# Kernel tuning notes

Measured on AMD Instinct MI355X. Metric: run time of the kernel, lower is better.

The kernel has to match this reference:

```python
import jax, jax.numpy as jnp
import numpy as np

S, B, I, H = 2048, 64, 128, 128
E = float(np.e)


def setup_inputs() -> dict:
    key = jax.random.key(0)
    ks = jax.random.split(key, 16)
    s = 1.0 / np.sqrt(H)
    inp = {
        "x": jax.random.normal(ks[0], (S, B, I), jnp.float32),
        "h0": jnp.zeros((2, B, H), jnp.float32),
        "c0": jnp.zeros((2, B, H), jnp.float32),
        # elapsed times, strictly positive
        "delta_ts": jax.random.uniform(ks[1], (B, S), jnp.float32, 0.1, 10.0),
    }
    names = ["W_ih", "W_hh", "b_ih", "b_hh", "W_d", "b_d"]
    shapes = [(4 * H, I), (4 * H, H), (4 * H,), (4 * H,), (H, H), (H,)]
    idx = 2
    for d in ["f", "r"]:
        for n, sh in zip(names, shapes):
            inp[f"{n}_{d}"] = jax.random.uniform(ks[idx], sh, jnp.float32, -s, s)
            idx += 1
    return inp


def _run_dir(x, dt, h, c, W_ih, W_hh, b_ih, b_hh, W_d, b_d):
    """Scan a TLSTM cell over time. x: [S,B,I], dt: [S,B]."""
    def step(carry, inp):
        h, c = carry
        xt, dtt = inp
        # time-aware memory decomposition (Baytas et al.)
        c_s = jnp.tanh(c @ W_d.T + b_d)               # short-term memory
        c_adj = c - c_s + c_s / jnp.log(E + dtt[:, None])  # discounted by elapsed time
        gates = xt @ W_ih.T + b_ih + h @ W_hh.T + b_hh
        i_g, f_g, g_g, o_g = jnp.split(gates, 4, axis=-1)
        c_n = jax.nn.sigmoid(f_g) * c_adj + jax.nn.sigmoid(i_g) * jnp.tanh(g_g)
        h_n = jax.nn.sigmoid(o_g) * jnp.tanh(c_n)
        return (h_n, c_n), h_n

    (h, c), ys = jax.lax.scan(step, (h, c), (x, dt))
    return ys, h, c


def reference(x, h0, c0, delta_ts,
              W_ih_f, W_hh_f, b_ih_f, b_hh_f, W_d_f, b_d_f,
              W_ih_r, W_hh_r, b_ih_r, b_hh_r, W_d_r, b_d_r):
    dt = delta_ts.T  # [S, B]
    out_f, _, _ = _run_dir(x, dt, h0[0], c0[0],
                           W_ih_f, W_hh_f, b_ih_f, b_hh_f, W_d_f, b_d_f)
    out_r, _, _ = _run_dir(x[::-1], dt[::-1], h0[1], c0[1],
                           W_ih_r, W_hh_r, b_ih_r, b_hh_r, W_d_r, b_d_r)
    return jnp.concatenate([out_f, out_r[::-1]], axis=-1)  # [S, B, 2H]
```

## Files before the change

kernel.cpp:

```cpp
#include <hip/hip_runtime.h>
#include <hip/hip_bf16.h>

#define SEQ  2048
#define BAT  64
#define HID  128
#define LDSP 136

#define XB_OFF  (1u << 20)
#define IL_OFF  (35u << 20)

typedef __bf16 bf16x8 __attribute__((ext_vector_type(8)));
typedef float  f32x4  __attribute__((ext_vector_type(4)));

#define MFMA(a,b,c) __builtin_amdgcn_mfma_f32_16x16x32_bf16((a),(b),(c),0,0,0)

__device__ __forceinline__ float sig_f(float x) {
    return __fdividef(1.0f, 1.0f + __expf(-x));
}
__device__ __forceinline__ float tanh_f(float x) {
    return 1.0f - __fdividef(2.0f, 1.0f + __expf(2.0f * x));
}
__device__ __forceinline__ bf16x8 cvt8(const float* p) {
    bf16x8 r;
    #pragma unroll
    for (int i = 0; i < 8; ++i) r[i] = (__bf16)p[i];
    return r;
}

__global__ void cvt_x_kernel(const float* __restrict__ x, __bf16* __restrict__ xb) {
    const int i = (blockIdx.x * 256 + threadIdx.x) * 4;
    const float4 v = *reinterpret_cast<const float4*>(x + i);
    __bf16 o[4];
    o[0] = (__bf16)v.x; o[1] = (__bf16)v.y; o[2] = (__bf16)v.z; o[3] = (__bf16)v.w;
    *reinterpret_cast<uint2*>(xb + i) = *reinterpret_cast<const uint2*>(o);
}

__global__ void prep_ilog_kernel(const float* __restrict__ dts, float* __restrict__ il) {
    const int idx = blockIdx.x * 256 + threadIdx.x;
    const int b = idx >> 11, t = idx & 2047;
    const float l = __logf(2.718281828459045f + dts[idx]);
    il[t * BAT + b] = __fdividef(1.0f, l) - 1.0f;
}

__global__ __launch_bounds__(512, 2) void tlstm_main(
    const __bf16* __restrict__ xb,   const float* __restrict__ ilg,
    const float* __restrict__ h0,    const float* __restrict__ c0,
    const float* __restrict__ Wih_f, const float* __restrict__ Whh_f,
    const float* __restrict__ bih_f, const float* __restrict__ bhh_f,
    const float* __restrict__ Wd_f,  const float* __restrict__ bd_f,
    const float* __restrict__ Wih_r, const float* __restrict__ Whh_r,
    const float* __restrict__ bih_r, const float* __restrict__ bhh_r,
    const float* __restrict__ Wd_r,  const float* __restrict__ bd_r,
    float* __restrict__ out)
{
    const int d    = blockIdx.x >> 4;
    const int b0   = (blockIdx.x & 15) * 4;
    const int tid  = threadIdx.x;
    const int w    = tid >> 6;
    const int lane = tid & 63;
    const int nl   = lane & 15;
    const int q    = lane >> 4;
    const int j    = w * 16 + nl;

    const float* Wih = d ? Wih_r : Wih_f;
    const float* Whh = d ? Whh_r : Whh_f;
    const float* bih = d ? bih_r : bih_f;
    const float* bhh = d ? bhh_r : bhh_f;
    const float* Wd  = d ? Wd_r  : Wd_f;
    const float* bd  = d ? bd_r  : bd_f;

    __shared__ __align__(16) __bf16 hc_a[2][16][LDSP];

    bf16x8 whh_fr[4][4], wih_fr[4][4], wd_fr[4];
    #pragma unroll
    for (int g = 0; g < 4; ++g) {
        const int row = g * 128 + j;
        #pragma unroll
        for (int kt = 0; kt < 4; ++kt) {
            const int off = row * HID + kt * 32 + q * 8;
            wih_fr[g][kt] = cvt8(Wih + off);
            whh_fr[g][kt] = cvt8(Whh + off);
        }
    }
    #pragma unroll
    for (int kt = 0; kt < 4; ++kt)
        wd_fr[kt] = cvt8(Wd + j * HID + kt * 32 + q * 8);

    float bias_g[4];
    #pragma unroll
    for (int g = 0; g < 4; ++g)
        bias_g[g] = bih[g * 128 + j] + bhh[g * 128 + j];
    const float bias_d = bd[j];

    for (int e = tid; e < 4 * HID; e += 512) {
        const int ci = e >> 7, k = e & 127;
        hc_a[0][ci * 4][k]     = (__bf16)h0[(d * BAT + b0 + ci) * HID + k];
        hc_a[0][ci * 4 + 1][k] = (__bf16)c0[(d * BAT + b0 + ci) * HID + k];
    }
    float c_st = c0[(d * BAT + b0 + q) * HID + j];
    __syncthreads();

    const int t0      = d ? (SEQ - 1) : 0;
    const int tstep   = d ? -1 : 1;
    const int xstride = tstep * BAT * HID;
    const int istride = tstep * BAT;
    const int ostride = tstep * BAT * 256;

    const __bf16* xp0 = xb + (size_t)((t0 + tstep * (nl & 3)) * BAT + b0 + (nl >> 2)) * HID + q * 8;
    const float*  ip0 = ilg + (size_t)t0 * BAT + b0 + q;
    float*        op  = out + (size_t)(t0 * BAT + b0 + q) * 256 + d * 128 + j;

    bf16x8 xfrA[4], xfrB[4];
    f32x4  xaccA[4], xaccB[4];
    float  ilA[4], ilB[4];

    {
        bf16x8 x0[4];
        #pragma unroll
        for (int kt = 0; kt < 4; ++kt)
            x0[kt] = *reinterpret_cast<const bf16x8*>(xp0 + kt * 32);
        #pragma unroll
        for (int g = 0; g < 4; ++g)
            xaccA[g] = f32x4{bias_g[g], bias_g[g], bias_g[g], bias_g[g]};
        #pragma unroll
        for (int kt = 0; kt < 4; ++kt) {
            xaccA[0] = MFMA(x0[kt], wih_fr[0][kt], xaccA[0]);
            xaccA[1] = MFMA(x0[kt], wih_fr[1][kt], xaccA[1]);
            xaccA[2] = MFMA(x0[kt], wih_fr[2][kt], xaccA[2]);
            xaccA[3] = MFMA(x0[kt], wih_fr[3][kt], xaccA[3]);
        }
    }
    #pragma unroll
    for (int kt = 0; kt < 4; ++kt)
        xfrA[kt] = *reinterpret_cast<const bf16x8*>(xp0 + 4 * xstride + kt * 32);
    #pragma unroll
    for (int dt = 0; dt < 4; ++dt)
        ilA[dt] = ip0[dt * istride];

    const __bf16* xpl = xp0 + 8 * xstride;
    const float*  ipl = ip0 + 4 * istride;

    auto window = [&](f32x4 (&xaccCur)[4], f32x4 (&xaccNext)[4],
                      bf16x8 (&xfrUse)[4], bf16x8 (&xfrLd)[4],
                      float (&ilCur)[4], float (&ilNext)[4]) __attribute__((always_inline)) {
        #pragma unroll
        for (int dt = 0; dt < 4; ++dt) {
            const int p = dt & 1;

            bf16x8 hcfr[4];
            #pragma unroll
            for (int kt = 0; kt < 4; ++kt)
                hcfr[kt] = *reinterpret_cast<const bf16x8*>(&hc_a[p][nl][kt * 32 + q * 8]);

            {
                const bf16x8 xf = xfrUse[dt];
                if (dt == 0) {
                    #pragma unroll
                    for (int g = 0; g < 4; ++g) {
                        const f32x4 binit = f32x4{bias_g[g], bias_g[g], bias_g[g], bias_g[g]};
                        xaccNext[g] = MFMA(xf, wih_fr[g][0], binit);
                    }
                } else {
                    #pragma unroll
                    for (int g = 0; g < 4; ++g)
                        xaccNext[g] = MFMA(xf, wih_fr[g][dt], xaccNext[g]);
                }
            }

            f32x4 ai, af, ag, ao;
            {
                const float s0 = xaccCur[0][dt], s1 = xaccCur[1][dt];
                const float s2 = xaccCur[2][dt], s3 = xaccCur[3][dt];
                ai = f32x4{s0, s0, s0, s0};
                af = f32x4{s1, s1, s1, s1};
                ag = f32x4{s2, s2, s2, s2};
                ao = f32x4{s3, s3, s3, s3};
            }
            f32x4 acs = f32x4{bias_d, bias_d, bias_d, bias_d};
            #pragma unroll
            for (int kt = 0; kt < 4; ++kt) {
                ai  = MFMA(hcfr[kt], whh_fr[0][kt], ai);
                af  = MFMA(hcfr[kt], whh_fr[1][kt], af);
                ag  = MFMA(hcfr[kt], whh_fr[2][kt], ag);
                ao  = MFMA(hcfr[kt], whh_fr[3][kt], ao);
                acs = MFMA(hcfr[kt], wd_fr[kt], acs);
            }

            xfrLd[dt]  = *reinterpret_cast<const bf16x8*>(xpl + dt * 32);
            ilNext[dt] = ipl[dt * istride];

            const int pn = p ^ 1;
            {
                const float cs   = tanh_f(acs[1]);
                const float cadj = fmaf(cs, ilCur[dt], c_st);
                const float gi   = sig_f(ai[0]);
                const float gf   = sig_f(af[0]);
                const float gg   = tanh_f(ag[0]);
                const float go   = sig_f(ao[0]);
                const float cn   = gf * cadj + gi * gg;
                const float hn   = go * tanh_f(cn);
                c_st = cn;
                hc_a[pn][q * 4][j]     = (__bf16)hn;
                hc_a[pn][q * 4 + 1][j] = (__bf16)cn;
                *op = hn;
            }
            op += ostride;

            asm volatile("s_waitcnt lgkmcnt(0)\n\ts_barrier" ::: "memory");
        }
        xpl += 4 * xstride;
        ipl += 4 * istride;
    };

    for (int wn = 0; wn < SEQ / 4; wn += 2) {
        window(xaccA, xaccB, xfrA, xfrB, ilA, ilB);
        window(xaccB, xaccA, xfrB, xfrA, ilB, ilA);
    }
}

extern "C" void kernel_launch(void* const* d_in, const int* in_sizes, int n_in,
                              void* d_out, int out_size, void* d_ws, size_t ws_size,
                              hipStream_t stream) {
    const float* x     = (const float*)d_in[0];
    const float* h0    = (const float*)d_in[1];
    const float* c0    = (const float*)d_in[2];
    const float* dts   = (const float*)d_in[3];
    const float* Wih_f = (const float*)d_in[4];
    const float* Whh_f = (const float*)d_in[5];
    const float* bih_f = (const float*)d_in[6];
    const float* bhh_f = (const float*)d_in[7];
    const float* Wd_f  = (const float*)d_in[8];
    const float* bd_f  = (const float*)d_in[9];
    const float* Wih_r = (const float*)d_in[10];
    const float* Whh_r = (const float*)d_in[11];
    const float* bih_r = (const float*)d_in[12];
    const float* bhh_r = (const float*)d_in[13];
    const float* Wd_r  = (const float*)d_in[14];
    const float* bd_r  = (const float*)d_in[15];
    float* out = (float*)d_out;

    __bf16* xbuf = (__bf16*)((char*)d_ws + XB_OFF);
    float*  il   = (float*)((char*)d_ws + IL_OFF);

    cvt_x_kernel<<<16384, 256, 0, stream>>>(x, xbuf);
    prep_ilog_kernel<<<512, 256, 0, stream>>>(dts, il);

    tlstm_main<<<32, 512, 0, stream>>>(xbuf, il, h0, c0,
                                       Wih_f, Whh_f, bih_f, bhh_f, Wd_f, bd_f,
                                       Wih_r, Whh_r, bih_r, bhh_r, Wd_r, bd_r,
                                       out);
}
```

Baseline: 2.279 ms.

## Compute input projection per chunk and rotate h/c rows across MFMA output lanes

The input-projection MFMAs for each 4-step chunk now run at the start of that chunk, no longer interleaved one window ahead. The full f32x4 accumulator is used directly as the gate init, so the per-step lane broadcasts go away. The h and c rows in the LDS staging buffer rotate positions each step, so each step's results land in a different accumulator lane. This drops the xacc double buffer and the scalar broadcast work, but the x-projection MFMAs now sit on the critical path at every chunk boundary instead of overlapping the recurrent ones.

Result: faster. 1.829 ms (-19.7%).

```diff
diff --git a/kernel.cpp b/kernel.cpp
--- a/kernel.cpp
+++ b/kernel.cpp
@@ -91,11 +91,12 @@
     for (int g = 0; g < 4; ++g)
         bias_g[g] = bih[g * 128 + j] + bhh[g * 128 + j];
     const float bias_d = bd[j];
+    const f32x4 bdv = f32x4{bias_d, bias_d, bias_d, bias_d};
 
     for (int e = tid; e < 4 * HID; e += 512) {
         const int ci = e >> 7, k = e & 127;
         hc_a[0][ci * 4][k]     = (__bf16)h0[(d * BAT + b0 + ci) * HID + k];
-        hc_a[0][ci * 4 + 1][k] = (__bf16)c0[(d * BAT + b0 + ci) * HID + k];
+        hc_a[0][ci * 4 + 2][k] = (__bf16)c0[(d * BAT + b0 + ci) * HID + k];
     }
     float c_st = c0[(d * BAT + b0 + q) * HID + j];
     __syncthreads();
@@ -111,72 +112,52 @@
     float*        op  = out + (size_t)(t0 * BAT + b0 + q) * 256 + d * 128 + j;
 
     bf16x8 xfrA[4], xfrB[4];
-    f32x4  xaccA[4], xaccB[4];
     float  ilA[4], ilB[4];
 
-    {
-        bf16x8 x0[4];
-        #pragma unroll
-        for (int kt = 0; kt < 4; ++kt)
-            x0[kt] = *reinterpret_cast<const bf16x8*>(xp0 + kt * 32);
-        #pragma unroll
-        for (int g = 0; g < 4; ++g)
-            xaccA[g] = f32x4{bias_g[g], bias_g[g], bias_g[g], bias_g[g]};
-        #pragma unroll
-        for (int kt = 0; kt < 4; ++kt) {
-            xaccA[0] = MFMA(x0[kt], wih_fr[0][kt], xaccA[0]);
-            xaccA[1] = MFMA(x0[kt], wih_fr[1][kt], xaccA[1]);
-            xaccA[2] = MFMA(x0[kt], wih_fr[2][kt], xaccA[2]);
-            xaccA[3] = MFMA(x0[kt], wih_fr[3][kt], xaccA[3]);
-        }
-    }
-    #pragma unroll
-    for (int kt = 0; kt < 4; ++kt)
-        xfrA[kt] = *reinterpret_cast<const bf16x8*>(xp0 + 4 * xstride + kt * 32);
-    #pragma unroll
-    for (int dt = 0; dt < 4; ++dt)
-        ilA[dt] = ip0[dt * istride];
-
+    #pragma unroll
+    for (int kt = 0; kt < 4; ++kt) {
+        xfrA[kt] = *reinterpret_cast<const bf16x8*>(xp0 + kt * 32);
+        xfrB[kt] = *reinterpret_cast<const bf16x8*>(xp0 + 4 * xstride + kt * 32);
+    }
+    #pragma unroll
+    for (int dtv = 0; dtv < 4; ++dtv) {
+        ilA[dtv] = ip0[dtv * istride];
+        ilB[dtv] = ip0[(4 + dtv) * istride];
+    }
     const __bf16* xpl = xp0 + 8 * xstride;
-    const float*  ipl = ip0 + 4 * istride;
-
-    auto window = [&](f32x4 (&xaccCur)[4], f32x4 (&xaccNext)[4],
-                      bf16x8 (&xfrUse)[4], bf16x8 (&xfrLd)[4],
-                      float (&ilCur)[4], float (&ilNext)[4]) __attribute__((always_inline)) {
+    const float*  ipl = ip0 + 8 * istride;
+
+    auto chunk = [&](bf16x8 (&xfrCur)[4], float (&ilCur)[4]) __attribute__((always_inline)) {
+        f32x4 xacc[4];
+        #pragma unroll
+        for (int g = 0; g < 4; ++g) {
+            const f32x4 bg = f32x4{bias_g[g], bias_g[g], bias_g[g], bias_g[g]};
+            xacc[g] = MFMA(xfrCur[0], wih_fr[g][0], bg);
+        }
+        #pragma unroll
+        for (int kt = 1; kt < 4; ++kt) {
+            xacc[0] = MFMA(xfrCur[kt], wih_fr[0][kt], xacc[0]);
+            xacc[1] = MFMA(xfrCur[kt], wih_fr[1][kt], xacc[1]);
+            xacc[2] = MFMA(xfrCur[kt], wih_fr[2][kt], xacc[2]);
+            xacc[3] = MFMA(xfrCur[kt], wih_fr[3][kt], xacc[3]);
+        }
+
         #pragma unroll
         for (int dt = 0; dt < 4; ++dt) {
-            const int p = dt & 1;
+            const int p  = dt & 1;
+            const int pn = p ^ 1;
+            const int hr = dt;
+            const int cr = (dt + 2) & 3;
+
+            const float il_use = ilCur[dt];
 
             bf16x8 hcfr[4];
             #pragma unroll
             for (int kt = 0; kt < 4; ++kt)
                 hcfr[kt] = *reinterpret_cast<const bf16x8*>(&hc_a[p][nl][kt * 32 + q * 8]);
 
-            {
-                const bf16x8 xf = xfrUse[dt];
-                if (dt == 0) {
-                    #pragma unroll
-                    for (int g = 0; g < 4; ++g) {
-                        const f32x4 binit = f32x4{bias_g[g], bias_g[g], bias_g[g], bias_g[g]};
-                        xaccNext[g] = MFMA(xf, wih_fr[g][0], binit);
-                    }
-                } else {
-                    #pragma unroll
-                    for (int g = 0; g < 4; ++g)
-                        xaccNext[g] = MFMA(xf, wih_fr[g][dt], xaccNext[g]);
-                }
-            }
-
-            f32x4 ai, af, ag, ao;
-            {
-                const float s0 = xaccCur[0][dt], s1 = xaccCur[1][dt];
-                const float s2 = xaccCur[2][dt], s3 = xaccCur[3][dt];
-                ai = f32x4{s0, s0, s0, s0};
-                af = f32x4{s1, s1, s1, s1};
-                ag = f32x4{s2, s2, s2, s2};
-                ao = f32x4{s3, s3, s3, s3};
-            }
-            f32x4 acs = f32x4{bias_d, bias_d, bias_d, bias_d};
+            f32x4 ai = xacc[0], af = xacc[1], ag = xacc[2], ao = xacc[3];
+            f32x4 acs = bdv;
             #pragma unroll
             for (int kt = 0; kt < 4; ++kt) {
                 ai  = MFMA(hcfr[kt], whh_fr[0][kt], ai);
@@ -186,22 +167,21 @@
                 acs = MFMA(hcfr[kt], wd_fr[kt], acs);
             }
 
-            xfrLd[dt]  = *reinterpret_cast<const bf16x8*>(xpl + dt * 32);
-            ilNext[dt] = ipl[dt * istride];
-
-            const int pn = p ^ 1;
+            xfrCur[dt] = *reinterpret_cast<const bf16x8*>(xpl + dt * 32);
+            ilCur[dt]  = ipl[dt * istride];
+
             {
-                const float cs   = tanh_f(acs[1]);
-                const float cadj = fmaf(cs, ilCur[dt], c_st);
-                const float gi   = sig_f(ai[0]);
-                const float gf   = sig_f(af[0]);
-                const float gg   = tanh_f(ag[0]);
-                const float go   = sig_f(ao[0]);
+                const float cs   = tanh_f(acs[cr]);
+                const float cadj = fmaf(cs, il_use, c_st);
+                const float gi   = sig_f(ai[hr]);
+                const float gf   = sig_f(af[hr]);
+                const float gg   = tanh_f(ag[hr]);
+                const float go   = sig_f(ao[hr]);
                 const float cn   = gf * cadj + gi * gg;
                 const float hn   = go * tanh_f(cn);
                 c_st = cn;
-                hc_a[pn][q * 4][j]     = (__bf16)hn;
-                hc_a[pn][q * 4 + 1][j] = (__bf16)cn;
+                hc_a[pn][q * 4 + ((dt + 1) & 3)][j] = (__bf16)hn;
+                hc_a[pn][q * 4 + ((dt + 3) & 3)][j] = (__bf16)cn;
                 *op = hn;
             }
             op += ostride;
@@ -212,9 +192,9 @@
         ipl += 4 * istride;
     };
 
-    for (int wn = 0; wn < SEQ / 4; wn += 2) {
-        window(xaccA, xaccB, xfrA, xfrB, ilA, ilB);
-        window(xaccB, xaccA, xfrB, xfrA, ilB, ilA);
+    for (int tc = 0; tc < SEQ / 4; tc += 2) {
+        chunk(xfrA, ilA);
+        chunk(xfrB, ilB);
     }
 }
 
```
